# Kernel tuning notes

Measured on AMD Instinct MI355X. Metric: run time of the kernel, lower is better.

Reference implementation:

```python
import jax, jax.numpy as jnp
import numpy as np

EPS = 1e-7
NORM_EPS = 1e-12  # matches torch F.normalize eps

def _l2_normalize(x, axis):
    n = jnp.linalg.norm(x, axis=axis, keepdims=True)
    return x / jnp.maximum(n, NORM_EPS)

def setup_inputs() -> dict:
    key = jax.random.key(0)
    k1, k2, k3 = jax.random.split(key, 3)
    B, D, C = 131072, 512, 2
    feat = jax.random.normal(k1, (B, D), dtype=jnp.float32)
    label = jax.random.randint(k2, (B,), 0, C, dtype=jnp.int64)
    # xavier_uniform for W of shape (C, D)
    limit = float(np.sqrt(6.0 / (C + D)))
    W = jax.random.uniform(k3, (C, D), dtype=jnp.float32, minval=-limit, maxval=limit)
    return {"feat": feat, "W": W, "label": label}

def reference(feat, W, label):
    s, m = 64.0, 0.5
    feat_n = _l2_normalize(feat, axis=1)          # [B, D]
    W_n = _l2_normalize(W, axis=1)                # [C, D]
    cos_theta = jnp.clip(feat_n @ W_n.T, -1.0 + EPS, 1.0 - EPS)  # [B, C]
    theta = jnp.arccos(cos_theta)
    cos_theta_m = jnp.cos(theta + m)
    one_hot = jax.nn.one_hot(label, W.shape[0], dtype=cos_theta.dtype)
    blended = cos_theta * (1.0 - one_hot) + cos_theta_m * one_hot
    return blended * s
```

## Files before the change

kernel.cpp:

```cpp
#include <hip/hip_runtime.h>
#include <math.h>


#define D_DIM 512

__device__ __forceinline__ float dot4(const float4& a, const float4& b) {
    return a.x * b.x + a.y * b.y + a.z * b.z + a.w * b.w;
}

__global__ __launch_bounds__(256, 4) void arcface_kernel(
    const float* __restrict__ feat,
    const float* __restrict__ W,
    const int* __restrict__ label,
    float* __restrict__ out,
    int n_rows)
{
    const float EPS   = 1e-7f;
    const float COS_M = 0.87758256189037271612f;
    const float SIN_M = 0.47942553860420300027f;
    const float S     = 64.0f;

    __shared__ float s_inv[2];

    const int tid  = threadIdx.x;
    const int wave = tid >> 6;
    const int lane = tid & 63;

    if (wave < 2) {
        const float4* Wv = (const float4*)(W + wave * D_DIM);
        float4 a = Wv[lane];
        float4 b = Wv[64 + lane];
        float ss = dot4(a, a) + dot4(b, b);
        #pragma unroll
        for (int m = 32; m >= 1; m >>= 1) ss += __shfl_xor(ss, m);
        if (lane == 0) {
            s_inv[wave] = 1.0f / fmaxf(sqrtf(ss), 1e-12f);
        }
    }
    __syncthreads();
    const float invW0 = s_inv[0];
    const float invW1 = s_inv[1];

    const float4* W0v = (const float4*)W;
    const float4* W1v = (const float4*)(W + D_DIM);
    const float4 w00 = W0v[lane];
    const float4 w01 = W0v[64 + lane];
    const float4 w10 = W1v[lane];
    const float4 w11 = W1v[64 + lane];

    const int gw      = blockIdx.x * 4 + wave;
    const int n_waves = gridDim.x * 4;

    for (int r = gw; r < n_rows; r += n_waves) {
        const float4* fv = (const float4*)(feat + (size_t)r * D_DIM);
        float4 f0 = fv[lane];
        float4 f1 = fv[64 + lane];

        float d0 = dot4(f0, w00) + dot4(f1, w01);
        float d1 = dot4(f0, w10) + dot4(f1, w11);
        float nn = dot4(f0, f0)  + dot4(f1, f1);

        #pragma unroll
        for (int m = 32; m >= 1; m >>= 1) {
            d0 += __shfl_xor(d0, m);
            d1 += __shfl_xor(d1, m);
            nn += __shfl_xor(nn, m);
        }

        if (lane == 0) {
            const float invF = 1.0f / fmaxf(sqrtf(nn), 1e-12f);
            float c0 = d0 * invF * invW0;
            float c1 = d1 * invF * invW1;
            c0 = fminf(fmaxf(c0, -1.0f + EPS), 1.0f - EPS);
            c1 = fminf(fmaxf(c1, -1.0f + EPS), 1.0f - EPS);
            const float m0 = c0 * COS_M - sqrtf(fmaxf(1.0f - c0 * c0, 0.0f)) * SIN_M;
            const float m1 = c1 * COS_M - sqrtf(fmaxf(1.0f - c1 * c1, 0.0f)) * SIN_M;
            const int lb = label[r];
            const float o0 = (lb == 0) ? m0 : c0;
            const float o1 = (lb == 1) ? m1 : c1;
            ((float2*)out)[r] = make_float2(o0 * S, o1 * S);
        }
    }
}

extern "C" void kernel_launch(void* const* d_in, const int* in_sizes, int n_in,
                              void* d_out, int out_size, void* d_ws, size_t ws_size,
                              hipStream_t stream) {
    const float* feat  = (const float*)d_in[0];
    const float* W     = (const float*)d_in[1];
    const int*   label = (const int*)d_in[2];
    float*       out   = (float*)d_out;

    const int n_rows = in_sizes[2];

    const int blocks = 4096;
    arcface_kernel<<<blocks, 256, 0, stream>>>(feat, W, label, out, n_rows);
}
```

Before: 358.4 us.

## Split waves into half-wave row workers with two rows in flight and prescaled W

Each 32-lane half-wave now owns a row, so a wave handles two rows at once. Each half-wave also loads two rows (A and B) per iteration so more memory requests are outstanding. W norms are computed per wave with shuffles and folded into the weight registers, which removes the shared-memory reduction and the __syncthreads. Register use roughly doubles for feature data, which may reduce occupancy under the launch bound of 4 blocks per CU.

```diff
diff --git a/kernel.cpp b/kernel.cpp
--- a/kernel.cpp
+++ b/kernel.cpp
@@ -6,6 +6,10 @@
 
 __device__ __forceinline__ float dot4(const float4& a, const float4& b) {
     return a.x * b.x + a.y * b.y + a.z * b.z + a.w * b.w;
+}
+
+__device__ __forceinline__ float4 scale4(const float4& a, float s) {
+    return make_float4(a.x * s, a.y * s, a.z * s, a.w * s);
 }
 
 __global__ __launch_bounds__(256, 4) void arcface_kernel(
@@ -20,65 +24,90 @@
     const float SIN_M = 0.47942553860420300027f;
     const float S     = 64.0f;
 
-    __shared__ float s_inv[2];
-
     const int tid  = threadIdx.x;
     const int wave = tid >> 6;
     const int lane = tid & 63;
-
-    if (wave < 2) {
-        const float4* Wv = (const float4*)(W + wave * D_DIM);
-        float4 a = Wv[lane];
-        float4 b = Wv[64 + lane];
-        float ss = dot4(a, a) + dot4(b, b);
-        #pragma unroll
-        for (int m = 32; m >= 1; m >>= 1) ss += __shfl_xor(ss, m);
-        if (lane == 0) {
-            s_inv[wave] = 1.0f / fmaxf(sqrtf(ss), 1e-12f);
-        }
-    }
-    __syncthreads();
-    const float invW0 = s_inv[0];
-    const float invW1 = s_inv[1];
+    const int l32  = lane & 31;
 
     const float4* W0v = (const float4*)W;
     const float4* W1v = (const float4*)(W + D_DIM);
-    const float4 w00 = W0v[lane];
-    const float4 w01 = W0v[64 + lane];
-    const float4 w10 = W1v[lane];
-    const float4 w11 = W1v[64 + lane];
+    float4 w0[4], w1[4];
+    #pragma unroll
+    for (int k = 0; k < 4; k++) {
+        w0[k] = W0v[l32 + 32 * k];
+        w1[k] = W1v[l32 + 32 * k];
+    }
 
-    const int gw      = blockIdx.x * 4 + wave;
-    const int n_waves = gridDim.x * 4;
+    float ss0 = 0.f, ss1 = 0.f;
+    #pragma unroll
+    for (int k = 0; k < 4; k++) {
+        ss0 += dot4(w0[k], w0[k]);
+        ss1 += dot4(w1[k], w1[k]);
+    }
+    #pragma unroll
+    for (int m = 16; m >= 1; m >>= 1) {
+        ss0 += __shfl_xor(ss0, m);
+        ss1 += __shfl_xor(ss1, m);
+    }
+    const float inv0 = 1.0f / fmaxf(sqrtf(ss0), 1e-12f);
+    const float inv1 = 1.0f / fmaxf(sqrtf(ss1), 1e-12f);
+    #pragma unroll
+    for (int k = 0; k < 4; k++) {
+        w0[k] = scale4(w0[k], inv0);
+        w1[k] = scale4(w1[k], inv1);
+    }
 
-    for (int r = gw; r < n_rows; r += n_waves) {
-        const float4* fv = (const float4*)(feat + (size_t)r * D_DIM);
-        float4 f0 = fv[lane];
-        float4 f1 = fv[64 + lane];
+    const int hw  = (blockIdx.x * 4 + wave) * 2 + (lane >> 5);
+    const int nhw = gridDim.x * 8;
 
-        float d0 = dot4(f0, w00) + dot4(f1, w01);
-        float d1 = dot4(f0, w10) + dot4(f1, w11);
-        float nn = dot4(f0, f0)  + dot4(f1, f1);
+    for (int r = hw; r < n_rows; r += 2 * nhw) {
+        const int  rA   = r;
+        const int  rB   = r + nhw;
+        const bool hasB = (rB < n_rows);
+
+        const float4* fA = (const float4*)(feat + (size_t)rA * D_DIM);
+        const float4* fB = (const float4*)(feat + (size_t)(hasB ? rB : rA) * D_DIM);
+        float4 a[4], b[4];
+        #pragma unroll
+        for (int k = 0; k < 4; k++) a[k] = fA[l32 + 32 * k];
+        #pragma unroll
+        for (int k = 0; k < 4; k++) b[k] = fB[l32 + 32 * k];
+
+        float d0A = 0.f, d1A = 0.f, nnA = 0.f;
+        float d0B = 0.f, d1B = 0.f, nnB = 0.f;
+        #pragma unroll
+        for (int k = 0; k < 4; k++) {
+            d0A += dot4(a[k], w0[k]);  d1A += dot4(a[k], w1[k]);  nnA += dot4(a[k], a[k]);
+            d0B += dot4(b[k], w0[k]);  d1B += dot4(b[k], w1[k]);  nnB += dot4(b[k], b[k]);
+        }
 
         #pragma unroll
-        for (int m = 32; m >= 1; m >>= 1) {
-            d0 += __shfl_xor(d0, m);
-            d1 += __shfl_xor(d1, m);
-            nn += __shfl_xor(nn, m);
+        for (int m = 16; m >= 1; m >>= 1) {
+            d0A += __shfl_xor(d0A, m);  d1A += __shfl_xor(d1A, m);  nnA += __shfl_xor(nnA, m);
+            d0B += __shfl_xor(d0B, m);  d1B += __shfl_xor(d1B, m);  nnB += __shfl_xor(nnB, m);
         }
 
-        if (lane == 0) {
-            const float invF = 1.0f / fmaxf(sqrtf(nn), 1e-12f);
-            float c0 = d0 * invF * invW0;
-            float c1 = d1 * invF * invW1;
-            c0 = fminf(fmaxf(c0, -1.0f + EPS), 1.0f - EPS);
-            c1 = fminf(fmaxf(c1, -1.0f + EPS), 1.0f - EPS);
-            const float m0 = c0 * COS_M - sqrtf(fmaxf(1.0f - c0 * c0, 0.0f)) * SIN_M;
-            const float m1 = c1 * COS_M - sqrtf(fmaxf(1.0f - c1 * c1, 0.0f)) * SIN_M;
-            const int lb = label[r];
-            const float o0 = (lb == 0) ? m0 : c0;
-            const float o1 = (lb == 1) ? m1 : c1;
-            ((float2*)out)[r] = make_float2(o0 * S, o1 * S);
+        if (l32 == 0) {
+            {
+                const float invF = 1.0f / fmaxf(sqrtf(nnA), 1e-12f);
+                float c0 = fminf(fmaxf(d0A * invF, -1.0f + EPS), 1.0f - EPS);
+                float c1 = fminf(fmaxf(d1A * invF, -1.0f + EPS), 1.0f - EPS);
+                const float m0 = c0 * COS_M - sqrtf(fmaxf(1.0f - c0 * c0, 0.0f)) * SIN_M;
+                const float m1 = c1 * COS_M - sqrtf(fmaxf(1.0f - c1 * c1, 0.0f)) * SIN_M;
+                const int lb = label[rA];
+                ((float2*)out)[rA] = make_float2(((lb == 0) ? m0 : c0) * S,
+                                                 ((lb == 1) ? m1 : c1) * S);
+            }
+            if (hasB) {
+                const float invF = 1.0f / fmaxf(sqrtf(nnB), 1e-12f);
+                float c0 = fminf(fmaxf(d0B * invF, -1.0f + EPS), 1.0f - EPS);
+                float c1 = fminf(fmaxf(d1B * invF, -1.0f + EPS), 1.0f - EPS);
+                const float m0 = c0 * COS_M - sqrtf(fmaxf(1.0f - c0 * c0, 0.0f)) * SIN_M;
+                const float m1 = c1 * COS_M - sqrtf(fmaxf(1.0f - c1 * c1, 0.0f)) * SIN_M;
+                const int lb = label[rB];
+                ((float2*)out)[rB] = make_float2(((lb == 0) ? m0 : c0) * S,
+                                                 ((lb == 1) ? m1 : c1) * S);
+            }
         }
     }
 }
```

Result: no change. 357.3 us (-0.3%).
